# Performance work log

Measured on AMD Instinct MI355X. Metric: run time of the kernel, lower is better.

## Reference

```python
import math
import jax, jax.numpy as jnp
import numpy as np

B, S, D, H = 1, 4096, 1024, 16
HD = D // H


def setup_inputs() -> dict:
    key = jax.random.key(0)
    ks = jax.random.split(key, 11)
    s = 0.02
    inp = {
        "q": jax.random.normal(ks[0], (B, S, D), jnp.float32),
        "k": jax.random.normal(ks[1], (B, S, D), jnp.float32),
        "v": jax.random.normal(ks[2], (B, S, D), jnp.float32),
        # causal boolean mask, broadcastable over [B, H, S, S]
        "mask": jnp.tril(jnp.ones((S, S), jnp.bool_))[None, None],
        "Wq": jax.random.normal(ks[3], (D, D), jnp.float32) * s,
        "bq": jnp.zeros((D,), jnp.float32),
        "Wk": jax.random.normal(ks[4], (D, D), jnp.float32) * s,
        "bk": jnp.zeros((D,), jnp.float32),
        "Wv": jax.random.normal(ks[5], (D, D), jnp.float32) * s,
        "bv": jnp.zeros((D,), jnp.float32),
        "Wo": jax.random.normal(ks[6], (D, D), jnp.float32) * s,
        "bo": jnp.zeros((D,), jnp.float32),
    }
    return inp


def reference(q, k, v, mask, Wq, bq, Wk, bk, Wv, bv, Wo, bo):
    # projections (torch Linear: x @ W.T + b; here W is stored already transposed)
    qp = (q @ Wq + bq).reshape(B, S, H, HD)
    kp = (k @ Wk + bk).reshape(B, S, H, HD)
    vp = (v @ Wv + bv).reshape(B, S, H, HD)
    # scores: [B, H, S, S]
    scores = jnp.einsum("bqhd,bkhd->bhqk", qp, kp) / math.sqrt(HD)
    scores = jnp.where(mask, scores, -jnp.inf)
    attn = jax.nn.softmax(scores, axis=-1)
    # context: [B, H, S, HD] -> [B, S, D]
    ctx = jnp.einsum("bhqk,bkhd->bqhd", attn, vp).reshape(B, S, D)
    return ctx @ Wo + bo
```

## Files before the change

kernel.cpp:

```cpp
#include <hip/hip_runtime.h>
#include <hip/hip_bf16.h>


#define S_LEN 4096
#define D_DIM 1024
#define NHEAD 16
#define HDIM  64

typedef __hip_bfloat16 bf16;
typedef __attribute__((ext_vector_type(8))) short bf16x8v;
typedef __attribute__((ext_vector_type(4))) float f32x4;
typedef __attribute__((ext_vector_type(2))) unsigned int u32x2;

#define MFMA16(a, b, c) __builtin_amdgcn_mfma_f32_16x16x32_bf16((a), (b), (c), 0, 0, 0)

#if __has_builtin(__builtin_amdgcn_exp2f)
#define EXP2F(x) __builtin_amdgcn_exp2f(x)
#else
#define EXP2F(x) exp2f(x)
#endif

#define QSCALE (0.125f * 1.4426950408889634f)

template<int N> struct IC { static constexpr int value = N; };

__device__ __forceinline__ void async_cp16(const void* g, void* l) {
    __builtin_amdgcn_global_load_lds(
        (const __attribute__((address_space(1))) unsigned int*)g,
        (__attribute__((address_space(3))) unsigned int*)l, 16, 0, 0);
}

__device__ __forceinline__ unsigned int cvtpk_bf16(float lo, float hi) {
    unsigned int r;
    asm("v_cvt_pk_bf16_f32 %0, %1, %2" : "=v"(r) : "v"(lo), "v"(hi));
    return r;
}

__global__ __launch_bounds__(256) void cvt_bf16_k(
    const float* __restrict__ x0, const float* __restrict__ x1,
    const float* __restrict__ x2,
    bf16* __restrict__ y0, bf16* __restrict__ y1, bf16* __restrict__ y2)
{
    const float* x = (blockIdx.z == 0) ? x0 : (blockIdx.z == 1) ? x1 : x2;
    bf16*       y = (blockIdx.z == 0) ? y0 : (blockIdx.z == 1) ? y1 : y2;
    const size_t i = ((size_t)blockIdx.x * 256 + threadIdx.x);
    const float4 v = ((const float4*)x)[i];
    union { bf16 h[4]; short4 s; } u;
    u.h[0] = __float2bfloat16(v.x);
    u.h[1] = __float2bfloat16(v.y);
    u.h[2] = __float2bfloat16(v.z);
    u.h[3] = __float2bfloat16(v.w);
    ((short4*)y)[i] = u.s;
}

__global__ __launch_bounds__(256) void transpose_cvt_k(
    const float* __restrict__ W0, const float* __restrict__ W1,
    const float* __restrict__ W2, const float* __restrict__ W3,
    bf16* __restrict__ T0, bf16* __restrict__ T1,
    bf16* __restrict__ T2, bf16* __restrict__ T3)
{
    const float* W = (blockIdx.z == 0) ? W0 : (blockIdx.z == 1) ? W1
                   : (blockIdx.z == 2) ? W2 : W3;
    bf16*       Wt = (blockIdx.z == 0) ? T0 : (blockIdx.z == 1) ? T1
                   : (blockIdx.z == 2) ? T2 : T3;
    __shared__ float t[32][33];
    const int bx = blockIdx.x << 5, by = blockIdx.y << 5;
    const int tx = threadIdx.x & 31, ty = threadIdx.x >> 5;
#pragma unroll
    for (int i = 0; i < 32; i += 8)
        t[ty + i][tx] = W[(size_t)(by + ty + i) * D_DIM + bx + tx];
    __syncthreads();
#pragma unroll
    for (int i = 0; i < 32; i += 8)
        Wt[(size_t)(bx + ty + i) * D_DIM + by + tx] = __float2bfloat16(t[tx][ty + i]);
}

struct GemmJob {
    const bf16* A; const bf16* Wt; const float* bias; void* out;
    int mode; float scale;
};

__global__ __launch_bounds__(256) void gemm_k(GemmJob j0, GemmJob j1, GemmJob j2)
{
    const GemmJob j = (blockIdx.z == 0) ? j0 : (blockIdx.z == 1) ? j1 : j2;
    const int K = D_DIM;
    const int bn = blockIdx.x << 6;
    const int bm = blockIdx.y << 7;
    const int tid = threadIdx.x;
    const int w = tid >> 6, lane = tid & 63;
    const int col = lane & 15, g = lane >> 4;
    const int wr = (w >> 1) << 6, wc = (w & 1) << 5;

    __shared__ bf16 As[128 * 64];
    __shared__ bf16 Bs[64 * 64];

    f32x4 acc[4][2];
#pragma unroll
    for (int i = 0; i < 4; ++i)
#pragma unroll
        for (int jj = 0; jj < 2; ++jj) acc[i][jj] = (f32x4){0.f, 0.f, 0.f, 0.f};

    for (int kb = 0; kb < K; kb += 64) {
        __syncthreads();
#pragma unroll
        for (int e = 0; e < 4; ++e) {
            const int lin = (e << 8) + tid;
            const int row = lin >> 3, kc = lin & 7;
            async_cp16(j.A + (size_t)(bm + row) * K + kb + (kc << 3), &As[lin << 3]);
        }
#pragma unroll
        for (int e = 0; e < 2; ++e) {
            const int lin = (e << 8) + tid;
            const int row = lin >> 3, kc = lin & 7;
            async_cp16(j.Wt + (size_t)(bn + row) * K + kb + (kc << 3), &Bs[lin << 3]);
        }
        __syncthreads();

#pragma unroll
        for (int s = 0; s < 2; ++s) {
            bf16x8v af[4], bfv[2];
#pragma unroll
            for (int i = 0; i < 4; ++i)
                af[i] = *(const bf16x8v*)&As[((wr + (i << 4) + col) << 6) + (s << 5) + (g << 3)];
#pragma unroll
            for (int jj = 0; jj < 2; ++jj)
                bfv[jj] = *(const bf16x8v*)&Bs[((wc + (jj << 4) + col) << 6) + (s << 5) + (g << 3)];
#pragma unroll
            for (int i = 0; i < 4; ++i)
#pragma unroll
                for (int jj = 0; jj < 2; ++jj)
                    acc[i][jj] = MFMA16(af[i], bfv[jj], acc[i][jj]);
        }
    }

#pragma unroll
    for (int i = 0; i < 4; ++i)
#pragma unroll
    for (int jj = 0; jj < 2; ++jj)
#pragma unroll
    for (int reg = 0; reg < 4; ++reg) {
        const int row = bm + wr + (i << 4) + (g << 2) + reg;
        const int cg  = bn + wc + (jj << 4) + col;
        const float vv = (acc[i][jj][reg] + j.bias[cg]) * j.scale;
        if (j.mode == 0)
            ((bf16*)j.out)[(((size_t)(cg >> 6)) * S_LEN + row) * HDIM + (cg & 63)] =
                __float2bfloat16(vv);
        else if (j.mode == 2)
            ((bf16*)j.out)[((size_t)(cg >> 6) * HDIM + (cg & 63)) * S_LEN + row] =
                __float2bfloat16(vv);
        else
            ((float*)j.out)[(size_t)row * D_DIM + cg] = vv;
    }
}

__global__ __launch_bounds__(256) void attn_mfma_k(
    const bf16* __restrict__ Qp, const bf16* __restrict__ Kp,
    const bf16* __restrict__ Vt, bf16* __restrict__ ctx,
    float* __restrict__ Opart, float* __restrict__ lpart, int mode)
{
    __shared__ bf16 Ks[2][4096];
    __shared__ bf16 Vs[2][4096];

    const int bid = blockIdx.x;
    const int h   = bid & 15;
    const int jid = bid >> 4;

    int qb, t0, nt, chunk;
    bool dosplit, hdiag;
    if (mode == 1) {
        if (jid < 16)      { qb = 31 - jid;        t0 = 2*qb - 30; nt = 32;        dosplit = true;  chunk = 1; hdiag = true;  }
        else if (jid < 32) { qb = 31 - (jid - 16); t0 = 0;         nt = 2*qb - 30; dosplit = true;  chunk = 0; hdiag = false; }
        else               { qb = 15 - (jid - 32); t0 = 0;         nt = 2*qb + 2;  dosplit = false; chunk = 0; hdiag = true;  }
    } else {
        qb = 31 - jid; t0 = 0; nt = 2*qb + 2; dosplit = false; chunk = 0; hdiag = true;
    }

    const int q0  = qb << 7;
    const int tid = threadIdx.x, w = tid >> 6, lane = tid & 63;
    const int col = lane & 15, g = lane >> 4;

    const bf16* Kh = Kp + (size_t)h * S_LEN * HDIM;
    const bf16* Vh = Vt + (size_t)h * HDIM * S_LEN;

    const int qrowA = q0 + (w << 4) + col;
    const int qrowB = qrowA + 64;
    const size_t qbaseA = ((size_t)h * S_LEN + qrowA) * HDIM + (g << 3);
    const size_t qbaseB = qbaseA + (size_t)64 * HDIM;
    const bf16x8v qfA0 = *(const bf16x8v*)(Qp + qbaseA);
    const bf16x8v qfA1 = *(const bf16x8v*)(Qp + qbaseA + 32);
    const bf16x8v qfB0 = *(const bf16x8v*)(Qp + qbaseB);
    const bf16x8v qfB1 = *(const bf16x8v*)(Qp + qbaseB + 32);

    float plA = 0.f, plB = 0.f;
    f32x4 accA[4], accB[4];
#pragma unroll
    for (int t = 0; t < 4; ++t) {
        accA[t] = (f32x4){0.f, 0.f, 0.f, 0.f};
        accB[t] = (f32x4){0.f, 0.f, 0.f, 0.f};
    }

    auto stage = [&](int buf, int kb) {
        const int kk0 = kb << 6;
#pragma unroll
        for (int e = 0; e < 2; ++e) {
            const int lin = (e << 8) + tid;
            const int t = lin >> 7, G = (lin >> 4) & 7, c = lin & 15;
            async_cp16(Kh + (size_t)(kk0 + (t << 4) + c) * HDIM + (G << 3),
                       &Ks[buf][lin << 3]);
            async_cp16(Vh + (size_t)((t << 4) + c) * S_LEN + kk0 + (G << 3),
                       &Vs[buf][lin << 3]);
        }
    };

    auto body = [&](auto mtag, int kb, int cur) {
        constexpr int MODE = decltype(mtag)::value;
        const int kk0 = kb << 6;
        const bf16* Kc = Ks[cur];
        const bf16* Vc = Vs[cur];

        f32x4 saA[4], saB[4];
#pragma unroll
        for (int t = 0; t < 4; ++t) {
            saA[t] = (f32x4){0.f, 0.f, 0.f, 0.f};
            saB[t] = (f32x4){0.f, 0.f, 0.f, 0.f};
        }
        __builtin_amdgcn_s_setprio(1);
#pragma unroll
        for (int t = 0; t < 4; ++t) {
            const bf16x8v kf0 = *(const bf16x8v*)&Kc[((t << 7) + (g << 4) + col) << 3];
            const bf16x8v kf1 = *(const bf16x8v*)&Kc[((t << 7) + 64 + (g << 4) + col) << 3];
            if (MODE != 2) {
                saA[t] = MFMA16(kf0, qfA0, saA[t]);
                saA[t] = MFMA16(kf1, qfA1, saA[t]);
            }
            saB[t] = MFMA16(kf0, qfB0, saB[t]);
            saB[t] = MFMA16(kf1, qfB1, saB[t]);
        }
        __builtin_amdgcn_s_setprio(0);

#pragma unroll
        for (int t = 0; t < 4; ++t) {
#pragma unroll
            for (int reg = 0; reg < 4; ++reg) {
                const int kidx = kk0 + (t << 4) + (g << 2) + reg;
                if (MODE != 2) {
                    float pA;
                    if (MODE == 1 && kidx > qrowA) pA = 0.f;
                    else                           pA = EXP2F(saA[t][reg]);
                    plA += pA; saA[t][reg] = pA;
                }
                float pB;
                if (MODE == 2 && kidx > qrowB) pB = 0.f;
                else                           pB = EXP2F(saB[t][reg]);
                plB += pB; saB[t][reg] = pB;
            }
        }

        union { unsigned int wd[4]; bf16x8v v; } pA0, pA1, pB0, pB1;
        if (MODE != 2) {
            unsigned int c0[4], c1[4];
#pragma unroll
            for (int t = 0; t < 4; ++t) {
                c0[t] = cvtpk_bf16(saA[t][0], saA[t][1]);
                c1[t] = cvtpk_bf16(saA[t][2], saA[t][3]);
            }
            u32x2 r0 = __builtin_amdgcn_permlane32_swap(c0[0], c0[1], false, false);
            u32x2 r1 = __builtin_amdgcn_permlane32_swap(c1[0], c1[1], false, false);
            u32x2 s0 = __builtin_amdgcn_permlane16_swap(r0[0], r0[1], false, false);
            u32x2 s1 = __builtin_amdgcn_permlane16_swap(r1[0], r1[1], false, false);
            pA0.wd[0] = s0[0]; pA0.wd[1] = s1[0]; pA0.wd[2] = s0[1]; pA0.wd[3] = s1[1];
            r0 = __builtin_amdgcn_permlane32_swap(c0[2], c0[3], false, false);
            r1 = __builtin_amdgcn_permlane32_swap(c1[2], c1[3], false, false);
            s0 = __builtin_amdgcn_permlane16_swap(r0[0], r0[1], false, false);
            s1 = __builtin_amdgcn_permlane16_swap(r1[0], r1[1], false, false);
            pA1.wd[0] = s0[0]; pA1.wd[1] = s1[0]; pA1.wd[2] = s0[1]; pA1.wd[3] = s1[1];
        }
        {
            unsigned int c0[4], c1[4];
#pragma unroll
            for (int t = 0; t < 4; ++t) {
                c0[t] = cvtpk_bf16(saB[t][0], saB[t][1]);
                c1[t] = cvtpk_bf16(saB[t][2], saB[t][3]);
            }
            u32x2 r0 = __builtin_amdgcn_permlane32_swap(c0[0], c0[1], false, false);
            u32x2 r1 = __builtin_amdgcn_permlane32_swap(c1[0], c1[1], false, false);
            u32x2 s0 = __builtin_amdgcn_permlane16_swap(r0[0], r0[1], false, false);
            u32x2 s1 = __builtin_amdgcn_permlane16_swap(r1[0], r1[1], false, false);
            pB0.wd[0] = s0[0]; pB0.wd[1] = s1[0]; pB0.wd[2] = s0[1]; pB0.wd[3] = s1[1];
            r0 = __builtin_amdgcn_permlane32_swap(c0[2], c0[3], false, false);
            r1 = __builtin_amdgcn_permlane32_swap(c1[2], c1[3], false, false);
            s0 = __builtin_amdgcn_permlane16_swap(r0[0], r0[1], false, false);
            s1 = __builtin_amdgcn_permlane16_swap(r1[0], r1[1], false, false);
            pB1.wd[0] = s0[0]; pB1.wd[1] = s1[0]; pB1.wd[2] = s0[1]; pB1.wd[3] = s1[1];
        }

        __builtin_amdgcn_s_setprio(1);
#pragma unroll
        for (int t = 0; t < 4; ++t) {
            const bf16x8v vf0 = *(const bf16x8v*)&Vc[((t << 7) + (g << 4) + col) << 3];
            const bf16x8v vf1 = *(const bf16x8v*)&Vc[((t << 7) + 64 + (g << 4) + col) << 3];
            if (MODE != 2) {
                accA[t] = MFMA16(vf0, pA0.v, accA[t]);
                accA[t] = MFMA16(vf1, pA1.v, accA[t]);
            }
            accB[t] = MFMA16(vf0, pB0.v, accB[t]);
            accB[t] = MFMA16(vf1, pB1.v, accB[t]);
        }
        __builtin_amdgcn_s_setprio(0);
    };

    int kb = t0, cur = 0;
    const int kend = t0 + nt;
    stage(0, kb);
    __syncthreads();

    const int nmain = hdiag ? nt - 2 : nt;
    for (int i = 0; i < nmain; ++i, ++kb) {
        if (kb + 1 < kend) stage(cur ^ 1, kb + 1);
        body(IC<0>{}, kb, cur);
        __syncthreads();
        cur ^= 1;
    }
    if (hdiag) {
        stage(cur ^ 1, kb + 1);
        body(IC<1>{}, kb, cur);
        __syncthreads();
        cur ^= 1; ++kb;
        body(IC<2>{}, kb, cur);
    }

    float lA = plA, lB = plB;
    lA += __shfl_xor(lA, 16); lA += __shfl_xor(lA, 32);
    lB += __shfl_xor(lB, 16); lB += __shfl_xor(lB, 32);

    if (!dosplit) {
        const float invA = 1.f / lA;
        const float invB = 1.f / lB;
#pragma unroll
        for (int t = 0; t < 4; ++t) {
            union { bf16 hh[4]; short4 s4; } uA, uB;
#pragma unroll
            for (int reg = 0; reg < 4; ++reg) {
                uA.hh[reg] = __float2bfloat16(accA[t][reg] * invA);
                uB.hh[reg] = __float2bfloat16(accB[t][reg] * invB);
            }
            *(short4*)&ctx[(size_t)qrowA * D_DIM + h * HDIM + (t << 4) + (g << 2)] = uA.s4;
            *(short4*)&ctx[(size_t)qrowB * D_DIM + h * HDIM + (t << 4) + (g << 2)] = uB.s4;
        }
    } else {
        const int srowA = ((qb - 16) << 7) + (w << 4) + col;
        const int srowB = srowA + 64;
        float* OpA = Opart + (((size_t)chunk * NHEAD + h) * 2048 + srowA) * HDIM;
        float* OpB = Opart + (((size_t)chunk * NHEAD + h) * 2048 + srowB) * HDIM;
#pragma unroll
        for (int t = 0; t < 4; ++t) {
            *(f32x4*)&OpA[(t << 4) + (g << 2)] = accA[t];
            *(f32x4*)&OpB[(t << 4) + (g << 2)] = accB[t];
        }
        if (g == 0) {
            lpart[((size_t)chunk * NHEAD + h) * 2048 + srowA] = lA;
            lpart[((size_t)chunk * NHEAD + h) * 2048 + srowB] = lB;
        }
    }
}

__global__ __launch_bounds__(256) void combine_k(
    const float* __restrict__ Opart, const float* __restrict__ lpart,
    bf16* __restrict__ ctx)
{
    const int tid = threadIdx.x;
    const int row = (blockIdx.x << 4) + (tid >> 4);
    const int d4  = (tid & 15) << 2;
    const int h   = row >> 11;
    const int srow = row & 2047;
    const float4 a = *(const float4*)&Opart[(size_t)row * HDIM + d4];
    const float4 b = *(const float4*)&Opart[(size_t)(32768 + row) * HDIM + d4];
    const float inv = 1.f / (lpart[row] + lpart[32768 + row]);
    union { bf16 hh[4]; short4 s4; } u;
    u.hh[0] = __float2bfloat16((a.x + b.x) * inv);
    u.hh[1] = __float2bfloat16((a.y + b.y) * inv);
    u.hh[2] = __float2bfloat16((a.z + b.z) * inv);
    u.hh[3] = __float2bfloat16((a.w + b.w) * inv);
    const int qrow = 2048 + srow;
    *(short4*)&ctx[(size_t)qrow * D_DIM + h * HDIM + d4] = u.s4;
}

extern "C" void kernel_launch(void* const* d_in, const int* in_sizes, int n_in,
                              void* d_out, int out_size, void* d_ws, size_t ws_size,
                              hipStream_t stream)
{
    const float* q  = (const float*)d_in[0];
    const float* k  = (const float*)d_in[1];
    const float* v  = (const float*)d_in[2];
    const float* Wq = (const float*)d_in[4];
    const float* bq = (const float*)d_in[5];
    const float* Wk = (const float*)d_in[6];
    const float* bk = (const float*)d_in[7];
    const float* Wv = (const float*)d_in[8];
    const float* bv = (const float*)d_in[9];
    const float* Wo = (const float*)d_in[10];
    const float* bo = (const float*)d_in[11];

    const size_t PE  = (size_t)S_LEN * D_DIM;
    const size_t WTE = (size_t)D_DIM * D_DIM;

    const dim3 tg(32, 32, 4);
    const dim3 gg(D_DIM / 64, S_LEN / 128, 1);
    const dim3 gg3(D_DIM / 64, S_LEN / 128, 3);
    const dim3 cg((unsigned)(PE / 1024), 1, 3);

    if (ws_size >= (size_t)64 * 1024 * 1024) {
        bf16* Qb = (bf16*)d_ws;
        bf16* Kb = Qb + PE;
        bf16* Vb = Kb + PE;
        bf16* Qp = Vb + PE;
        bf16* Kp = Qp + PE;
        bf16* Vt = Kp + PE;
        bf16* Wtq = Vt + PE;
        bf16* Wtk = Wtq + WTE;
        bf16* Wtv = Wtk + WTE;
        bf16* Wto = Wtv + WTE;
        bf16* ctx = Qb;
        float* Opart = (float*)Kb;
        float* lpart = (float*)(Wto + WTE);

        transpose_cvt_k<<<tg, 256, 0, stream>>>(Wq, Wk, Wv, Wo, Wtq, Wtk, Wtv, Wto);
        cvt_bf16_k<<<cg, 256, 0, stream>>>(q, k, v, Qb, Kb, Vb);

        GemmJob jq{Qb, Wtq, bq, Qp, 0, QSCALE};
        GemmJob jk{Kb, Wtk, bk, Kp, 0, 1.0f};
        GemmJob jv{Vb, Wtv, bv, Vt, 2, 1.0f};
        gemm_k<<<gg3, 256, 0, stream>>>(jq, jk, jv);

        attn_mfma_k<<<dim3(768), 256, 0, stream>>>(Qp, Kp, Vt, ctx, Opart, lpart, 1);
        combine_k<<<dim3(2048), 256, 0, stream>>>(Opart, lpart, ctx);

        GemmJob jo{ctx, Wto, bo, d_out, 1, 1.0f};
        gemm_k<<<gg, 256, 0, stream>>>(jo, jo, jo);
    } else {
        bf16* X  = (bf16*)d_ws;
        bf16* Qp = X + PE;
        bf16* Kp = Qp + PE;
        bf16* Vt = Kp + PE;
        bf16* Wtq = Vt + PE;
        bf16* Wtk = Wtq + WTE;
        bf16* Wtv = Wtk + WTE;
        bf16* Wto = Wtv + WTE;

        transpose_cvt_k<<<tg, 256, 0, stream>>>(Wq, Wk, Wv, Wo, Wtq, Wtk, Wtv, Wto);

        const dim3 cg1((unsigned)(PE / 1024), 1, 1);
        cvt_bf16_k<<<cg1, 256, 0, stream>>>(q, q, q, X, X, X);
        GemmJob jq{X, Wtq, bq, Qp, 0, QSCALE};
        gemm_k<<<gg, 256, 0, stream>>>(jq, jq, jq);
        cvt_bf16_k<<<cg1, 256, 0, stream>>>(k, k, k, X, X, X);
        GemmJob jk{X, Wtk, bk, Kp, 0, 1.0f};
        gemm_k<<<gg, 256, 0, stream>>>(jk, jk, jk);
        cvt_bf16_k<<<cg1, 256, 0, stream>>>(v, v, v, X, X, X);
        GemmJob jv{X, Wtv, bv, Vt, 2, 1.0f};
        gemm_k<<<gg, 256, 0, stream>>>(jv, jv, jv);

        attn_mfma_k<<<dim3(512), 256, 0, stream>>>(Qp, Kp, Vt, X, nullptr, nullptr, 0);

        GemmJob jo{X, Wto, bo, d_out, 1, 1.0f};
        gemm_k<<<gg, 256, 0, stream>>>(jo, jo, jo);
    }
}
```

Measured before the change: 302.5 us.

## Double-buffer GEMM shared-memory tiles and remap block indices for locality

The projection GEMM now keeps two shared-memory buffers for the A and W tiles and issues the next k-tile's async copies before running the MFMAs on the current tile. This overlaps global loads with compute and drops one barrier per iteration. Block indices are also remapped with a stride-8 interleave, which changes how tiles are spread across XCDs to improve L2 reuse. In exchange the kernel uses twice the LDS, which may reduce occupancy. Correctness depends on async_cp16 completing before the barrier and on the tile count dividing evenly by 8.

```diff
diff --git a/kernel.cpp b/kernel.cpp
--- a/kernel.cpp
+++ b/kernel.cpp
@@ -84,15 +84,21 @@
 {
     const GemmJob j = (blockIdx.z == 0) ? j0 : (blockIdx.z == 1) ? j1 : j2;
     const int K = D_DIM;
-    const int bn = blockIdx.x << 6;
-    const int bm = blockIdx.y << 7;
+
+    const int nx  = gridDim.x;
+    const int lin = blockIdx.y * nx + blockIdx.x;
+    const int per = (nx * gridDim.y) >> 3;
+    const int bmn = (lin & 7) * per + (lin >> 3);
+    const int bn = (bmn % nx) << 6;
+    const int bm = (bmn / nx) << 7;
+
     const int tid = threadIdx.x;
     const int w = tid >> 6, lane = tid & 63;
     const int col = lane & 15, g = lane >> 4;
     const int wr = (w >> 1) << 6, wc = (w & 1) << 5;
 
-    __shared__ bf16 As[128 * 64];
-    __shared__ bf16 Bs[64 * 64];
+    __shared__ bf16 As[2][128 * 64];
+    __shared__ bf16 Bs[2][64 * 64];
 
     f32x4 acc[4][2];
 #pragma unroll
@@ -100,37 +106,46 @@
 #pragma unroll
         for (int jj = 0; jj < 2; ++jj) acc[i][jj] = (f32x4){0.f, 0.f, 0.f, 0.f};
 
+    auto stage = [&](int buf, int kb) {
+#pragma unroll
+        for (int e = 0; e < 4; ++e) {
+            const int l2 = (e << 8) + tid;
+            const int row = l2 >> 3, kc = l2 & 7;
+            async_cp16(j.A + (size_t)(bm + row) * K + kb + (kc << 3), &As[buf][l2 << 3]);
+        }
+#pragma unroll
+        for (int e = 0; e < 2; ++e) {
+            const int l2 = (e << 8) + tid;
+            const int row = l2 >> 3, kc = l2 & 7;
+            async_cp16(j.Wt + (size_t)(bn + row) * K + kb + (kc << 3), &Bs[buf][l2 << 3]);
+        }
+    };
+
+    stage(0, 0);
+    __syncthreads();
+    int cur = 0;
+
     for (int kb = 0; kb < K; kb += 64) {
-        __syncthreads();
-#pragma unroll
-        for (int e = 0; e < 4; ++e) {
-            const int lin = (e << 8) + tid;
-            const int row = lin >> 3, kc = lin & 7;
-            async_cp16(j.A + (size_t)(bm + row) * K + kb + (kc << 3), &As[lin << 3]);
-        }
-#pragma unroll
-        for (int e = 0; e < 2; ++e) {
-            const int lin = (e << 8) + tid;
-            const int row = lin >> 3, kc = lin & 7;
-            async_cp16(j.Wt + (size_t)(bn + row) * K + kb + (kc << 3), &Bs[lin << 3]);
-        }
-        __syncthreads();
+        if (kb + 64 < K) stage(cur ^ 1, kb + 64);
 
 #pragma unroll
         for (int s = 0; s < 2; ++s) {
             bf16x8v af[4], bfv[2];
 #pragma unroll
             for (int i = 0; i < 4; ++i)
-                af[i] = *(const bf16x8v*)&As[((wr + (i << 4) + col) << 6) + (s << 5) + (g << 3)];
+                af[i] = *(const bf16x8v*)&As[cur][((wr + (i << 4) + col) << 6) + (s << 5) + (g << 3)];
 #pragma unroll
             for (int jj = 0; jj < 2; ++jj)
-                bfv[jj] = *(const bf16x8v*)&Bs[((wc + (jj << 4) + col) << 6) + (s << 5) + (g << 3)];
+                bfv[jj] = *(const bf16x8v*)&Bs[cur][((wc + (jj << 4) + col) << 6) + (s << 5) + (g << 3)];
 #pragma unroll
             for (int i = 0; i < 4; ++i)
 #pragma unroll
                 for (int jj = 0; jj < 2; ++jj)
                     acc[i][jj] = MFMA16(af[i], bfv[jj], acc[i][jj]);
         }
+
+        __syncthreads();
+        cur ^= 1;
     }
 
 #pragma unroll
```

After: 307.3 us. About the same (+1.6%).
